# Performance work log

Hardware: AMD Instinct MI355X
Metric: run time of the kernel (lower is better)

The kernel has to match this reference:

```python
import jax, jax.numpy as jnp
import numpy as np

DIM = 256
HEADS = 4
HEAD_DIM = DIM // HEADS
SCALE = HEAD_DIM ** -0.5


def setup_inputs() -> dict:
    key = jax.random.key(0)
    ks = jax.random.split(key, 9)
    B, N, C = 2, 4096, DIM
    x = jax.random.normal(ks[0], (B, N, C), dtype=jnp.float32)
    # xavier-uniform-ish init for square weights
    lim = np.sqrt(6.0 / (C + C)).astype(np.float32)
    def w(k):
        return jax.random.uniform(k, (C, C), dtype=jnp.float32, minval=-lim, maxval=lim)
    return {
        "x": x,
        "Wq": w(ks[1]), "bq": jnp.zeros((C,), jnp.float32),
        "Wk": w(ks[2]), "bk": jnp.zeros((C,), jnp.float32),
        "Wv": w(ks[3]), "bv": jnp.zeros((C,), jnp.float32),
        "Wo": w(ks[4]), "bo": jnp.zeros((C,), jnp.float32),
    }


def reference(x, Wq, bq, Wk, bk, Wv, bv, Wo, bo):
    B, N, C = x.shape
    x = jnp.clip(x, -10000.0, 10000.0)
    # projections (torch Linear: x @ W.T + b), then split heads -> [B, H, N, D]
    def heads(t):
        return t.reshape(B, N, HEADS, HEAD_DIM).transpose(0, 2, 1, 3)
    q = heads((x @ Wq.T + bq).astype(jnp.float32))
    k = heads((x @ Wk.T + bk).astype(jnp.float32))
    v = heads((x @ Wv.T + bv).astype(jnp.float32))
    # naive full attention: [B, H, N, N] scores materialized (as in source)
    attn = jnp.einsum("bhnd,bhmd->bhnm", q, k) * SCALE
    attn = jax.nn.softmax(attn, axis=-1)
    out = jnp.einsum("bhnm,bhmd->bhnd", attn, v)
    out = out.transpose(0, 2, 1, 3).reshape(B, N, C)
    # source casts to bf16 before the fp32 out_proj: emulate the precision loss
    out = out.astype(jnp.bfloat16).astype(jnp.float32)
    return out @ Wo.T + bo
```

## Files before the change

kernel.cpp:

```cpp
#include <hip/hip_runtime.h>
#include <hip/hip_bf16.h>

typedef unsigned short ushort_t;
typedef unsigned int u32;
typedef __bf16 bf16x4 __attribute__((ext_vector_type(4)));
typedef __bf16 bf16x8 __attribute__((ext_vector_type(8)));
typedef float f32x4 __attribute__((ext_vector_type(4)));
typedef float f32x16 __attribute__((ext_vector_type(16)));

#define DIMC 256
#define NSEQ 4096
#define BATCH 2
#define NHEADS 4
#define HDIM 64
#define QK_SCALE_LOG2E 0.18033688011112042f

__device__ __forceinline__ ushort_t f2bf(float f) {
    __bf16 b = (__bf16)f;
    return *(ushort_t*)&b;
}
__device__ __forceinline__ float clip1e4(float x) {
    return fminf(fmaxf(x, -10000.f), 10000.f);
}
__device__ __forceinline__ void gload_lds16(const void* g, void* l) {
    __builtin_amdgcn_global_load_lds((const __attribute__((address_space(1))) u32*)g,
                                     (__attribute__((address_space(3))) u32*)l, 16, 0, 0);
}

__global__ __launch_bounds__(256)
void qkv_proj_kernel(const float* __restrict__ xg,
                     const float* __restrict__ Wq, const float* __restrict__ bq,
                     const float* __restrict__ Wk, const float* __restrict__ bk,
                     const float* __restrict__ Wv, const float* __restrict__ bv,
                     ushort_t* __restrict__ Qg, ushort_t* __restrict__ Kg,
                     ushort_t* __restrict__ Vtg)
{
    __shared__ __attribute__((aligned(16))) ushort_t Ash[128][72];
    __shared__ __attribute__((aligned(16))) ushort_t Bsh[64][72];
    const int tid = threadIdx.x;
    const int lane = tid & 63;
    const int wv = tid >> 6;
    const int c16 = lane & 15;
    const int g = lane >> 4;

    const int bx = blockIdx.x;
    const int rowbase = blockIdx.y * 128;
    const int t = bx >> 2;
    const int cw = (bx & 3) * 64;

    const float* Wg = (t == 0) ? Wq : (t == 1) ? Wk : Wv;
    const float* bg = (t == 0) ? bq : (t == 1) ? bk : bv;
    const float cscale = (t == 0) ? QK_SCALE_LOG2E : 1.0f;

    const f32x4 zero = {0.f, 0.f, 0.f, 0.f};
    f32x4 acc[2][4];
#pragma unroll
    for (int a = 0; a < 2; ++a)
#pragma unroll
        for (int b = 0; b < 4; ++b) acc[a][b] = zero;

    for (int kt = 0; kt < 4; ++kt) {
        const int kb = kt * 64;
#pragma unroll
        for (int i = 0; i < 8; ++i) {
            int idx = tid + i * 256;
            int row = idx >> 4, c4 = (idx & 15) * 4;
            const float4 v = *(const float4*)&xg[(rowbase + row) * DIMC + kb + c4];
            bf16x4 pk;
            pk[0] = (__bf16)clip1e4(v.x); pk[1] = (__bf16)clip1e4(v.y);
            pk[2] = (__bf16)clip1e4(v.z); pk[3] = (__bf16)clip1e4(v.w);
            *(bf16x4*)&Ash[row][c4] = pk;
        }
#pragma unroll
        for (int i = 0; i < 4; ++i) {
            int idx = tid + i * 256;
            int row = idx >> 4, c4 = (idx & 15) * 4;
            const float4 v = *(const float4*)&Wg[(cw + row) * DIMC + kb + c4];
            bf16x4 pk;
            pk[0] = (__bf16)v.x; pk[1] = (__bf16)v.y;
            pk[2] = (__bf16)v.z; pk[3] = (__bf16)v.w;
            *(bf16x4*)&Bsh[row][c4] = pk;
        }
        __syncthreads();
#pragma unroll
        for (int ks = 0; ks < 2; ++ks) {
            bf16x8 a0 = *(const bf16x8*)&Ash[wv * 32 + c16][ks * 32 + g * 8];
            bf16x8 a1 = *(const bf16x8*)&Ash[wv * 32 + 16 + c16][ks * 32 + g * 8];
#pragma unroll
            for (int j = 0; j < 4; ++j) {
                bf16x8 bfr = *(const bf16x8*)&Bsh[j * 16 + c16][ks * 32 + g * 8];
                acc[0][j] = __builtin_amdgcn_mfma_f32_16x16x32_bf16(a0, bfr, acc[0][j], 0, 0, 0);
                acc[1][j] = __builtin_amdgcn_mfma_f32_16x16x32_bf16(a1, bfr, acc[1][j], 0, 0, 0);
            }
        }
        __syncthreads();
    }
    if (t < 2) {
        ushort_t* outg = (t == 0) ? Qg : Kg;
#pragma unroll
        for (int j = 0; j < 4; ++j) {
            int col = cw + j * 16 + c16;
            float bias = bg[col];
            int h = col >> 6, d = col & 63;
#pragma unroll
            for (int fr = 0; fr < 2; ++fr) {
#pragma unroll
                for (int r = 0; r < 4; ++r) {
                    int row = rowbase + wv * 32 + fr * 16 + g * 4 + r;
                    int b = row >> 12, n = row & (NSEQ - 1);
                    float val = (acc[fr][j][r] + bias) * cscale;
                    outg[(((b * NHEADS + h) * NSEQ) + n) * HDIM + d] = f2bf(val);
                }
            }
        }
    } else {
#pragma unroll
        for (int j = 0; j < 4; ++j) {
            int col = cw + j * 16 + c16;
            float bias = bg[col];
            int h = col >> 6, d = col & 63;
#pragma unroll
            for (int fr = 0; fr < 2; ++fr) {
                int row0 = rowbase + wv * 32 + fr * 16 + g * 4;
                int b = row0 >> 12, n0 = row0 & (NSEQ - 1);
                bf16x4 pk;
#pragma unroll
                for (int r = 0; r < 4; ++r) pk[r] = (__bf16)(acc[fr][j][r] + bias);
                *(bf16x4*)&Vtg[(((size_t)(b * NHEADS + h) << 6) + d) * NSEQ + n0] = pk;
            }
        }
    }
}

__global__ __launch_bounds__(256)
void attn_kernel(const ushort_t* __restrict__ Qg, const ushort_t* __restrict__ Kg,
                 const ushort_t* __restrict__ Vtg, ushort_t* __restrict__ AOg)
{
    __shared__ __attribute__((aligned(16))) ushort_t Ksh[2][64][64];
    __shared__ __attribute__((aligned(16))) ushort_t Vsh[3][64][64];
    __shared__ __attribute__((aligned(16))) ushort_t Psh[2][64][64];
    __shared__ float Lsh[2][64];
    const int tid = threadIdx.x;
    const int lane = tid & 63;
    const int w = tid >> 6;
    const int l31 = lane & 31;
    const int hi = lane >> 5;
    const int qh = w & 1;
    const int kh = w >> 1;
    const int bh = blockIdx.x;
    const int qbase = blockIdx.y * 64;
    const int sub = lane >> 3, ch = lane & 7;

    bf16x8 qf[4];
    const int qrow = qbase + 32 * qh + l31;
#pragma unroll
    for (int m = 0; m < 4; ++m)
        qf[m] = *(const bf16x8*)&Qg[((bh * NSEQ + qrow) << 6) + 16 * m + hi * 8];

    f32x16 o;
#pragma unroll
    for (int r = 0; r < 16; ++r) o[r] = 0.f;
    float lsum = 0.f;

    auto stageK = [&](int t, int buf) {
#pragma unroll
        for (int i = 0; i < 2; ++i) {
            int row = w * 16 + i * 8 + sub;
            int chs = ch ^ (row & 7);
            gload_lds16(&Kg[((bh * NSEQ + t * 64 + row) << 6) + chs * 8],
                        &Ksh[buf][w * 16 + i * 8][0]);
        }
    };
    auto stageV = [&](int t, int buf) {
#pragma unroll
        for (int i = 0; i < 2; ++i) {
            int row = w * 16 + i * 8 + sub;
            int chs = ch ^ (row & 7);
            gload_lds16(&Vtg[((bh << 6) + row) * NSEQ + t * 64 + chs * 8],
                        &Vsh[buf][w * 16 + i * 8][0]);
        }
    };

    stageK(0, 0);
    stageV(0, 0);
    __syncthreads();

    const int NT = NSEQ / 64;
    for (int t = 0; t < NT; ++t) {
        if (t + 1 < NT) { stageK(t + 1, (t + 1) & 1); stageV(t + 1, (t + 1) % 3); }
        __builtin_amdgcn_sched_barrier(0);

        f32x16 s;
#pragma unroll
        for (int r = 0; r < 16; ++r) s[r] = 0.f;
        {
            const int row = 32 * kh + l31;
            const int sw = row & 7;
#pragma unroll
            for (int m = 0; m < 4; ++m) {
                bf16x8 kf = *(const bf16x8*)&Ksh[t & 1][row][((2 * m + hi) ^ sw) * 8];
                s = __builtin_amdgcn_mfma_f32_32x32x16_bf16(kf, qf[m], s, 0, 0, 0);
            }
        }

        if (t > 0) {
            const int vb = (t - 1) % 3, pb = (t - 1) & 1;
            const int prow = 32 * qh + l31;
            const int psw = prow & 7;
            const int vrow = 32 * kh + l31;
            const int vsw = vrow & 7;
#pragma unroll
            for (int m = 0; m < 4; ++m) {
                bf16x8 pa = *(const bf16x8*)&Psh[pb][prow][((2 * m + hi) ^ psw) * 8];
                bf16x8 vf = *(const bf16x8*)&Vsh[vb][vrow][((2 * m + hi) ^ vsw) * 8];
                o = __builtin_amdgcn_mfma_f32_32x32x16_bf16(pa, vf, o, 0, 0, 0);
            }
        }

        {
            const int pq = 32 * qh + l31;
            const int psw = pq & 7;
#pragma unroll
            for (int rg = 0; rg < 4; ++rg) {
                bf16x4 pk;
#pragma unroll
                for (int rr = 0; rr < 4; ++rr) {
                    float p = exp2f(s[4 * rg + rr]);
                    lsum += p;
                    pk[rr] = (__bf16)p;
                }
                *(bf16x4*)&Psh[t & 1][pq][((4 * kh + rg) ^ psw) * 8 + 4 * hi] = pk;
            }
        }
        __syncthreads();
    }

    {
        const int vb = (NT - 1) % 3, pb = (NT - 1) & 1;
        const int prow = 32 * qh + l31;
        const int psw = prow & 7;
        const int vrow = 32 * kh + l31;
        const int vsw = vrow & 7;
#pragma unroll
        for (int m = 0; m < 4; ++m) {
            bf16x8 pa = *(const bf16x8*)&Psh[pb][prow][((2 * m + hi) ^ psw) * 8];
            bf16x8 vf = *(const bf16x8*)&Vsh[vb][vrow][((2 * m + hi) ^ vsw) * 8];
            o = __builtin_amdgcn_mfma_f32_32x32x16_bf16(pa, vf, o, 0, 0, 0);
        }
    }

    lsum += __shfl_xor(lsum, 32, 64);
    if (hi == 0) Lsh[kh][32 * qh + l31] = lsum;
    __syncthreads();

    const int b = bh >> 2, h = bh & 3;
    const int dcol = h * HDIM + 32 * kh + l31;
#pragma unroll
    for (int rg = 0; rg < 4; ++rg) {
#pragma unroll
        for (int rr = 0; rr < 4; ++rr) {
            int q = rr + 8 * rg + 4 * hi + 32 * qh;
            float inv = 1.0f / (Lsh[0][q] + Lsh[1][q]);
            int n = qbase + q;
            AOg[(b * NSEQ + n) * DIMC + dcol] = f2bf(o[4 * rg + rr] * inv);
        }
    }
}

__global__ __launch_bounds__(256)
void oproj_kernel(const ushort_t* __restrict__ AOg, const float* __restrict__ Wo,
                  const float* __restrict__ bo, float* __restrict__ outg)
{
    __shared__ __attribute__((aligned(16))) ushort_t Ash[128][72];
    __shared__ __attribute__((aligned(16))) ushort_t Bsh[64][72];
    const int tid = threadIdx.x;
    const int lane = tid & 63;
    const int wv = tid >> 6;
    const int c16 = lane & 15;
    const int g = lane >> 4;
    const int cw = blockIdx.x * 64;
    const int rowbase = blockIdx.y * 128;

    const f32x4 zero = {0.f, 0.f, 0.f, 0.f};
    f32x4 acc[2][4];
#pragma unroll
    for (int a = 0; a < 2; ++a)
#pragma unroll
        for (int b = 0; b < 4; ++b) acc[a][b] = zero;

    for (int kt = 0; kt < 4; ++kt) {
        const int kb = kt * 64;
#pragma unroll
        for (int i = 0; i < 4; ++i) {
            int idx = tid + i * 256;
            int row = idx >> 3, d8 = (idx & 7) * 8;
            *(uint4*)&Ash[row][d8] = *(const uint4*)&AOg[(rowbase + row) * DIMC + kb + d8];
        }
#pragma unroll
        for (int i = 0; i < 4; ++i) {
            int idx = tid + i * 256;
            int row = idx >> 4, c4 = (idx & 15) * 4;
            const float4 v = *(const float4*)&Wo[(cw + row) * DIMC + kb + c4];
            bf16x4 pk;
            pk[0] = (__bf16)v.x; pk[1] = (__bf16)v.y;
            pk[2] = (__bf16)v.z; pk[3] = (__bf16)v.w;
            *(bf16x4*)&Bsh[row][c4] = pk;
        }
        __syncthreads();
#pragma unroll
        for (int ks = 0; ks < 2; ++ks) {
            bf16x8 a0 = *(const bf16x8*)&Ash[wv * 32 + c16][ks * 32 + g * 8];
            bf16x8 a1 = *(const bf16x8*)&Ash[wv * 32 + 16 + c16][ks * 32 + g * 8];
#pragma unroll
            for (int j = 0; j < 4; ++j) {
                bf16x8 bfr = *(const bf16x8*)&Bsh[j * 16 + c16][ks * 32 + g * 8];
                acc[0][j] = __builtin_amdgcn_mfma_f32_16x16x32_bf16(a0, bfr, acc[0][j], 0, 0, 0);
                acc[1][j] = __builtin_amdgcn_mfma_f32_16x16x32_bf16(a1, bfr, acc[1][j], 0, 0, 0);
            }
        }
        __syncthreads();
    }
#pragma unroll
    for (int j = 0; j < 4; ++j) {
        int col = cw + j * 16 + c16;
        float bias = bo[col];
#pragma unroll
        for (int fr = 0; fr < 2; ++fr) {
#pragma unroll
            for (int r = 0; r < 4; ++r) {
                int row = rowbase + wv * 32 + fr * 16 + g * 4 + r;
                outg[row * DIMC + col] = acc[fr][j][r] + bias;
            }
        }
    }
}

extern "C" void kernel_launch(void* const* d_in, const int* in_sizes, int n_in,
                              void* d_out, int out_size, void* d_ws, size_t ws_size,
                              hipStream_t stream)
{
    const float* x  = (const float*)d_in[0];
    const float* Wq = (const float*)d_in[1];
    const float* bq = (const float*)d_in[2];
    const float* Wk = (const float*)d_in[3];
    const float* bk = (const float*)d_in[4];
    const float* Wv = (const float*)d_in[5];
    const float* bv = (const float*)d_in[6];
    const float* Wo = (const float*)d_in[7];
    const float* bo = (const float*)d_in[8];
    float* out = (float*)d_out;

    ushort_t* ws = (ushort_t*)d_ws;
    const size_t SZ = (size_t)BATCH * NHEADS * NSEQ * HDIM;
    ushort_t* Qg  = ws;
    ushort_t* Kg  = ws + SZ;
    ushort_t* Vtg = ws + 2 * SZ;
    ushort_t* AOg = ws + 3 * SZ;

    qkv_proj_kernel<<<dim3(12, 64), 256, 0, stream>>>(x, Wq, bq, Wk, bk, Wv, bv, Qg, Kg, Vtg);
    attn_kernel<<<dim3(8, 64), 256, 0, stream>>>(Qg, Kg, Vtg, AOg);
    oproj_kernel<<<dim3(4, 64), 256, 0, stream>>>(AOg, Wo, bo, out);
}
```

Baseline: 165.4 us.

## Split attention KV range across two blocks and keep P in registers

Splits the key sequence into two halves over a new grid dimension, so each block writes unnormalized partial outputs and row sums, and the o-proj kernel combines them and normalizes. Within a block, P is now packed with cvt_pk_bf16 and permlane32_swap straight into MFMA operands instead of going through shared memory. The two waves that hold different key halves reduce their outputs through LDS before writing. The intent is more blocks in flight and fewer LDS round trips and barriers. In exchange it adds extra partial-output traffic and merge work in the o-proj kernel. It also relies on softmax without max subtraction and on bf16 partial sums.

```diff
diff --git a/kernel.cpp b/kernel.cpp
--- a/kernel.cpp
+++ b/kernel.cpp
@@ -132,14 +132,16 @@
     }
 }
 
-__global__ __launch_bounds__(256)
+__global__ __launch_bounds__(256, 4)
 void attn_kernel(const ushort_t* __restrict__ Qg, const ushort_t* __restrict__ Kg,
-                 const ushort_t* __restrict__ Vtg, ushort_t* __restrict__ AOg)
+                 const ushort_t* __restrict__ Vtg, ushort_t* __restrict__ Op,
+                 float* __restrict__ Lg)
 {
-    __shared__ __attribute__((aligned(16))) ushort_t Ksh[2][64][64];
-    __shared__ __attribute__((aligned(16))) ushort_t Vsh[3][64][64];
-    __shared__ __attribute__((aligned(16))) ushort_t Psh[2][64][64];
+    __shared__ __attribute__((aligned(16))) ushort_t pool[16384];
     __shared__ float Lsh[2][64];
+    ushort_t* Kpool = pool;
+    ushort_t* Vpool = pool + 8192;
+
     const int tid = threadIdx.x;
     const int lane = tid & 63;
     const int w = tid >> 6;
@@ -149,6 +151,7 @@
     const int kh = w >> 1;
     const int bh = blockIdx.x;
     const int qbase = blockIdx.y * 64;
+    const int split = blockIdx.z;
     const int sub = lane >> 3, ch = lane & 7;
 
     bf16x8 qf[4];
@@ -157,119 +160,125 @@
     for (int m = 0; m < 4; ++m)
         qf[m] = *(const bf16x8*)&Qg[((bh * NSEQ + qrow) << 6) + 16 * m + hi * 8];
 
-    f32x16 o;
-#pragma unroll
-    for (int r = 0; r < 16; ++r) o[r] = 0.f;
+    f32x16 o[2];
+#pragma unroll
+    for (int n = 0; n < 2; ++n)
+#pragma unroll
+        for (int r = 0; r < 16; ++r) o[n][r] = 0.f;
     float lsum = 0.f;
 
-    auto stageK = [&](int t, int buf) {
+    auto stageK = [&](int ta, int buf) {
 #pragma unroll
         for (int i = 0; i < 2; ++i) {
             int row = w * 16 + i * 8 + sub;
             int chs = ch ^ (row & 7);
-            gload_lds16(&Kg[((bh * NSEQ + t * 64 + row) << 6) + chs * 8],
-                        &Ksh[buf][w * 16 + i * 8][0]);
+            gload_lds16(&Kg[((bh * NSEQ + ta * 64 + row) << 6) + chs * 8],
+                        &Kpool[(buf * 64 + w * 16 + i * 8) * 64]);
         }
     };
-    auto stageV = [&](int t, int buf) {
+    auto stageV = [&](int ta, int buf) {
 #pragma unroll
         for (int i = 0; i < 2; ++i) {
             int row = w * 16 + i * 8 + sub;
             int chs = ch ^ (row & 7);
-            gload_lds16(&Vtg[((bh << 6) + row) * NSEQ + t * 64 + chs * 8],
-                        &Vsh[buf][w * 16 + i * 8][0]);
+            gload_lds16(&Vtg[((bh << 6) + row) * NSEQ + ta * 64 + chs * 8],
+                        &Vpool[(buf * 64 + w * 16 + i * 8) * 64]);
         }
     };
 
-    stageK(0, 0);
-    stageV(0, 0);
+    const int t0 = split * 32;
+    stageK(t0, 0);
+    stageV(t0, 0);
     __syncthreads();
 
-    const int NT = NSEQ / 64;
-    for (int t = 0; t < NT; ++t) {
-        if (t + 1 < NT) { stageK(t + 1, (t + 1) & 1); stageV(t + 1, (t + 1) % 3); }
+    for (int t = 0; t < 32; ++t) {
+        const int cur = t & 1;
+        if (t + 1 < 32) { stageK(t0 + t + 1, cur ^ 1); stageV(t0 + t + 1, cur ^ 1); }
         __builtin_amdgcn_sched_barrier(0);
 
         f32x16 s;
 #pragma unroll
         for (int r = 0; r < 16; ++r) s[r] = 0.f;
         {
-            const int row = 32 * kh + l31;
-            const int sw = row & 7;
+            const int krow = 32 * kh + l31, ksw = krow & 7;
 #pragma unroll
             for (int m = 0; m < 4; ++m) {
-                bf16x8 kf = *(const bf16x8*)&Ksh[t & 1][row][((2 * m + hi) ^ sw) * 8];
+                bf16x8 kf = *(const bf16x8*)&Kpool[(cur * 64 + krow) * 64 + ((2 * m + hi) ^ ksw) * 8];
                 s = __builtin_amdgcn_mfma_f32_32x32x16_bf16(kf, qf[m], s, 0, 0, 0);
             }
         }
 
-        if (t > 0) {
-            const int vb = (t - 1) % 3, pb = (t - 1) & 1;
-            const int prow = 32 * qh + l31;
-            const int psw = prow & 7;
-            const int vrow = 32 * kh + l31;
-            const int vsw = vrow & 7;
-#pragma unroll
-            for (int m = 0; m < 4; ++m) {
-                bf16x8 pa = *(const bf16x8*)&Psh[pb][prow][((2 * m + hi) ^ psw) * 8];
-                bf16x8 vf = *(const bf16x8*)&Vsh[vb][vrow][((2 * m + hi) ^ vsw) * 8];
-                o = __builtin_amdgcn_mfma_f32_32x32x16_bf16(pa, vf, o, 0, 0, 0);
-            }
-        }
-
-        {
-            const int pq = 32 * qh + l31;
-            const int psw = pq & 7;
-#pragma unroll
-            for (int rg = 0; rg < 4; ++rg) {
-                bf16x4 pk;
-#pragma unroll
-                for (int rr = 0; rr < 4; ++rr) {
-                    float p = exp2f(s[4 * rg + rr]);
-                    lsum += p;
-                    pk[rr] = (__bf16)p;
-                }
-                *(bf16x4*)&Psh[t & 1][pq][((4 * kh + rg) ^ psw) * 8 + 4 * hi] = pk;
-            }
-        }
-        __syncthreads();
-    }
-
-    {
-        const int vb = (NT - 1) % 3, pb = (NT - 1) & 1;
-        const int prow = 32 * qh + l31;
-        const int psw = prow & 7;
-        const int vrow = 32 * kh + l31;
-        const int vsw = vrow & 7;
-#pragma unroll
-        for (int m = 0; m < 4; ++m) {
-            bf16x8 pa = *(const bf16x8*)&Psh[pb][prow][((2 * m + hi) ^ psw) * 8];
-            bf16x8 vf = *(const bf16x8*)&Vsh[vb][vrow][((2 * m + hi) ^ vsw) * 8];
-            o = __builtin_amdgcn_mfma_f32_32x32x16_bf16(pa, vf, o, 0, 0, 0);
-        }
+        u32 WA[4], WB[4];
+#pragma unroll
+        for (int g = 0; g < 4; ++g) {
+            float e0 = exp2f(s[4 * g + 0]), e1 = exp2f(s[4 * g + 1]);
+            float e2 = exp2f(s[4 * g + 2]), e3 = exp2f(s[4 * g + 3]);
+            lsum += (e0 + e1) + (e2 + e3);
+            asm("v_cvt_pk_bf16_f32 %0, %1, %2" : "=v"(WA[g]) : "v"(e0), "v"(e1));
+            asm("v_cvt_pk_bf16_f32 %0, %1, %2" : "=v"(WB[g]) : "v"(e2), "v"(e3));
+        }
+
+#pragma unroll
+        for (int m = 0; m < 2; ++m) {
+            u32 a = WA[2 * m], b2 = WA[2 * m + 1];
+            u32 c = WB[2 * m], d2 = WB[2 * m + 1];
+            asm volatile("v_permlane32_swap_b32 %0, %1" : "+v"(a), "+v"(b2));
+            asm volatile("v_permlane32_swap_b32 %0, %1" : "+v"(c), "+v"(d2));
+            union { u32 u[4]; bf16x8 v; } pf;
+            pf.u[0] = a; pf.u[1] = c; pf.u[2] = b2; pf.u[3] = d2;
+#pragma unroll
+            for (int n = 0; n < 2; ++n) {
+                int vrow = 32 * n + l31;
+                bf16x8 vf = *(const bf16x8*)
+                    &Vpool[(cur * 64 + vrow) * 64 + ((4 * kh + 2 * m + hi) ^ (vrow & 7)) * 8];
+                o[n] = __builtin_amdgcn_mfma_f32_32x32x16_bf16(pf.v, vf, o[n], 0, 0, 0);
+            }
+        }
+        __syncthreads();
     }
 
     lsum += __shfl_xor(lsum, 32, 64);
     if (hi == 0) Lsh[kh][32 * qh + l31] = lsum;
+    float* Red = (float*)pool;
+    const int rbase = (qh * 64 + lane) * 34;
+    if (kh == 1) {
+#pragma unroll
+        for (int n = 0; n < 2; ++n)
+#pragma unroll
+            for (int j = 0; j < 8; ++j) {
+                float2 r; r.x = o[n][2 * j]; r.y = o[n][2 * j + 1];
+                *(float2*)&Red[rbase + n * 16 + 2 * j] = r;
+            }
+    }
     __syncthreads();
-
-    const int b = bh >> 2, h = bh & 3;
-    const int dcol = h * HDIM + 32 * kh + l31;
-#pragma unroll
-    for (int rg = 0; rg < 4; ++rg) {
-#pragma unroll
-        for (int rr = 0; rr < 4; ++rr) {
-            int q = rr + 8 * rg + 4 * hi + 32 * qh;
-            float inv = 1.0f / (Lsh[0][q] + Lsh[1][q]);
-            int n = qbase + q;
-            AOg[(b * NSEQ + n) * DIMC + dcol] = f2bf(o[4 * rg + rr] * inv);
+    if (kh == 0) {
+        const int b = bh >> 2, h = bh & 3;
+#pragma unroll
+        for (int n = 0; n < 2; ++n)
+#pragma unroll
+            for (int j = 0; j < 8; ++j) {
+                float2 r = *(const float2*)&Red[rbase + n * 16 + 2 * j];
+                o[n][2 * j] += r.x; o[n][2 * j + 1] += r.y;
+            }
+#pragma unroll
+        for (int n = 0; n < 2; ++n)
+#pragma unroll
+            for (int reg = 0; reg < 16; ++reg) {
+                int q = (reg & 3) + 8 * (reg >> 2) + 4 * hi + 32 * qh;
+                Op[((size_t)(split * BATCH + b) * NSEQ + qbase + q) * DIMC
+                   + h * HDIM + 32 * n + l31] = f2bf(o[n][reg]);
+            }
+        if (hi == 0) {
+            int q = 32 * qh + l31;
+            Lg[(split * 8 + bh) * NSEQ + qbase + q] = Lsh[0][q] + Lsh[1][q];
         }
     }
 }
 
 __global__ __launch_bounds__(256)
-void oproj_kernel(const ushort_t* __restrict__ AOg, const float* __restrict__ Wo,
-                  const float* __restrict__ bo, float* __restrict__ outg)
+void oproj_kernel(const ushort_t* __restrict__ Op, const float* __restrict__ Lg,
+                  const float* __restrict__ Wo, const float* __restrict__ bo,
+                  float* __restrict__ outg)
 {
     __shared__ __attribute__((aligned(16))) ushort_t Ash[128][72];
     __shared__ __attribute__((aligned(16))) ushort_t Bsh[64][72];
@@ -293,8 +302,18 @@
 #pragma unroll
         for (int i = 0; i < 4; ++i) {
             int idx = tid + i * 256;
-            int row = idx >> 3, d8 = (idx & 7) * 8;
-            *(uint4*)&Ash[row][d8] = *(const uint4*)&AOg[(rowbase + row) * DIMC + kb + d8];
+            int row = idx >> 3, ch8 = (idx & 7) * 8;
+            int grow = rowbase + row;
+            int b = grow >> 12, n = grow & (NSEQ - 1);
+            float l = Lg[(b * 4 + kt) * NSEQ + n] + Lg[(8 + b * 4 + kt) * NSEQ + n];
+            float inv = 1.0f / l;
+            bf16x8 O0 = *(const bf16x8*)&Op[((size_t)b * NSEQ + n) * DIMC + kb + ch8];
+            bf16x8 O1 = *(const bf16x8*)&Op[((size_t)(BATCH + b) * NSEQ + n) * DIMC + kb + ch8];
+            bf16x8 pk;
+#pragma unroll
+            for (int e = 0; e < 8; ++e)
+                pk[e] = (__bf16)(((float)O0[e] + (float)O1[e]) * inv);
+            *(bf16x8*)&Ash[row][ch8] = pk;
         }
 #pragma unroll
         for (int i = 0; i < 4; ++i) {
@@ -355,9 +374,10 @@
     ushort_t* Qg  = ws;
     ushort_t* Kg  = ws + SZ;
     ushort_t* Vtg = ws + 2 * SZ;
-    ushort_t* AOg = ws + 3 * SZ;
+    ushort_t* Op  = ws + 3 * SZ;
+    float*    Lg  = (float*)(ws + 5 * SZ);
 
     qkv_proj_kernel<<<dim3(12, 64), 256, 0, stream>>>(x, Wq, bq, Wk, bk, Wv, bv, Qg, Kg, Vtg);
-    attn_kernel<<<dim3(8, 64), 256, 0, stream>>>(Qg, Kg, Vtg, AOg);
-    oproj_kernel<<<dim3(4, 64), 256, 0, stream>>>(AOg, Wo, bo, out);
-}
+    attn_kernel<<<dim3(8, 64, 2), 256, 0, stream>>>(Qg, Kg, Vtg, Op, Lg);
+    oproj_kernel<<<dim3(4, 64), 256, 0, stream>>>(Op, Lg, Wo, bo, out);
+}
```

Measured after the change: 154.8 us. 6.4% less time.
